# Kernel tuning notes

Measured on AMD Instinct MI355X. Metric: run time of the kernel, lower is better.

Reference implementation:

```python
import jax, jax.numpy as jnp
import numpy as np

SCORE_THRESHOLD = 0.5
GRID = 512  # spatial extent per axis; batch in {0,1} so keys fit int32
SENTINEL = np.int32(2 ** 30)  # larger than any real key (< 2**28)


def _encode(coords):
    # coords: [N,4] int32 (batch, x, y, z) -> unique int32 key
    c = coords.astype(jnp.int32)
    return ((c[:, 0] * GRID + c[:, 1]) * GRID + c[:, 2]) * GRID + c[:, 3]


def _decode_np(k):
    z = k % GRID; k = k // GRID
    y = k % GRID; k = k // GRID
    x = k % GRID; b = k // GRID
    return np.stack([b, x, y, z], axis=1).astype(np.int32)


def setup_inputs() -> dict:
    rng = np.random.default_rng(0)
    Nx, Nm, Dx = 2_000_000, 2_000_000, 16
    # draw unique coordinate keys (MinkowskiEngine coords are unique per tensor)
    keys = np.unique(rng.integers(0, 2 * GRID ** 3, size=3 * Nx, dtype=np.int64)).astype(np.int32)
    rng.shuffle(keys)
    x_keys = keys[:Nx]
    m_keys = np.concatenate([x_keys[: Nm // 2], keys[Nx: Nx + Nm - Nm // 2]])
    rng.shuffle(m_keys)
    key = jax.random.key(0)
    k1, k2 = jax.random.split(key)
    return {
        "x_C": jnp.asarray(_decode_np(x_keys)),
        "x_F": jax.random.normal(k1, (Nx, Dx), dtype=jnp.float32),
        "m_C": jnp.asarray(_decode_np(m_keys)),
        "m_F": jax.random.uniform(k2, (Nm, 1), dtype=jnp.float32),
    }


def _gather_on_union(keys, feats, union_keys):
    # scatter each tensor's features onto the union coordinate set (zeros elsewhere)
    n = keys.shape[0]
    order = jnp.argsort(keys)
    ks = keys[order]
    fs = feats[order]
    pos = jnp.searchsorted(ks, union_keys)
    pc = jnp.clip(pos, 0, n - 1)
    found = (pos < n) & (ks[pc] == union_keys)
    return jnp.where(found[:, None], fs[pc], jnp.zeros((), feats.dtype))


def reference(x_C, x_F, m_C, m_F):
    Nx, Nm = x_F.shape[0], m_F.shape[0]
    xk = _encode(x_C)
    mk = _encode(m_C)
    # coordinate union (ME sparse-tensor addition); fixed size Nx+Nm, padded w/ sentinel
    uk = jnp.unique(jnp.concatenate([xk, mk]), size=Nx + Nm, fill_value=SENTINEL)
    xf = _gather_on_union(xk, x_F, uk)   # x features on union coords  [Nu, Dx]
    mf = _gather_on_union(mk, m_F, uk)   # mask scores on union coords [Nu, 1]
    # target = score above threshold AND x has any positive feature at this coord
    target = (mf[:, 0] > SCORE_THRESHOLD) & (xf > 0).any(axis=1)
    # prune expressed as fixed-shape masking (padding rows have target=False)
    return xf * target[:, None].astype(xf.dtype)
```

## Files before the change

kernel.cpp:

```cpp
#include <hip/hip_runtime.h>
#include <hip/hip_bf16.h>
#include <stdint.h>

#define KEYSPACE     (1u << 28)
#define NBUCKET      2048u
#define BUCKET_KEYS  (KEYSPACE / NBUCKET)
#define BUCKET_WORDS (BUCKET_KEYS / 16u)
#define BUCKET_CAP   4096u
#define EPB          16384
#define UMASK        0x55555555u
#define RECS_CAP     1024u

__device__ __forceinline__ uint32_t encode4(int4 c) {
    return ((((uint32_t)c.x * 512u + (uint32_t)c.y) * 512u + (uint32_t)c.z) * 512u) + (uint32_t)c.w;
}

__global__ __launch_bounds__(256) void bin_keys(const int* __restrict__ xC,
                                                const int* __restrict__ mC,
                                                const float* __restrict__ mF,
                                                uint2* __restrict__ barr,
                                                uint32_t* __restrict__ bcnt,
                                                int Nx, int Nm) {
    __shared__ uint32_t hist[NBUCKET];
    __shared__ uint32_t base[NBUCKET];
    int t = threadIdx.x;
    int total = Nx + Nm;
    int start = blockIdx.x * EPB;
    int end = min(start + EPB, total);

    for (int q = t; q < (int)NBUCKET; q += 256) hist[q] = 0u;
    __syncthreads();

    for (int e = start + t; e < end; e += 256) {
        uint32_t k = (e < Nx) ? encode4(reinterpret_cast<const int4*>(xC)[e])
                              : encode4(reinterpret_cast<const int4*>(mC)[e - Nx]);
        atomicAdd(&hist[k >> 17], 1u);
    }
    __syncthreads();

    for (int q = t; q < (int)NBUCKET; q += 256) {
        uint32_t h = hist[q];
        base[q] = h ? atomicAdd(&bcnt[q], h) : 0u;
        hist[q] = 0u;
    }
    __syncthreads();

    for (int e = start + t; e < end; e += 256) {
        uint32_t k; uint2 pl;
        if (e < Nx) {
            k = encode4(reinterpret_cast<const int4*>(xC)[e]);
            pl.x = (k & (BUCKET_KEYS - 1u)) | (1u << 18);
            pl.y = (uint32_t)e;
        } else {
            int j = e - Nx;
            k = encode4(reinterpret_cast<const int4*>(mC)[j]);
            pl.x = (k & (BUCKET_KEYS - 1u)) | ((mF[j] > 0.5f) ? (1u << 17) : 0u);
            pl.y = 0u;
        }
        uint32_t b = k >> 17;
        uint32_t pos = base[b] + atomicAdd(&hist[b], 1u);
        barr[(size_t)b * BUCKET_CAP + pos] = pl;
    }
}

__global__ __launch_bounds__(256) void build_bucket(const uint2* __restrict__ barr,
                                                    const uint32_t* __restrict__ bcnt,
                                                    uint2* __restrict__ records,
                                                    uint32_t* __restrict__ rcount,
                                                    uint32_t* __restrict__ Btot) {
    __shared__ uint32_t bmp[BUCKET_WORDS];
    __shared__ uint32_t gpre[512];
    __shared__ uint32_t sdata[256];
    __shared__ uint2 recs[RECS_CAP];
    __shared__ uint32_t nrec, rbase;
    int t = threadIdx.x;
    uint32_t b = blockIdx.x;

    {
        uint4 z = make_uint4(0u, 0u, 0u, 0u);
        uint4* bz = reinterpret_cast<uint4*>(bmp);
        for (int q = t; q < (int)(BUCKET_WORDS / 4u); q += 256) bz[q] = z;
    }
    __syncthreads();

    uint32_t n = bcnt[b];
    const uint2* ba = barr + (size_t)b * BUCKET_CAP;

    for (uint32_t e = t; e < n; e += 256u) {
        uint32_t pl = ba[e].x;
        uint32_t off = pl & (BUCKET_KEYS - 1u);
        uint32_t bits = 1u | (((pl >> 17) & 1u) << 1);
        atomicOr(&bmp[off >> 4], bits << ((off & 15u) * 2u));
    }
    __syncthreads();

    uint32_t c0 = 0u, c1 = 0u;
    {
        const uint32_t* w0 = bmp + (2 * t) * 16;
        const uint32_t* w1 = bmp + (2 * t + 1) * 16;
#pragma unroll
        for (int q = 0; q < 16; ++q) c0 += __popc(w0[q] & UMASK);
#pragma unroll
        for (int q = 0; q < 16; ++q) c1 += __popc(w1[q] & UMASK);
    }
    uint32_t s = c0 + c1;
    sdata[t] = s;
    __syncthreads();
    for (int off = 1; off < 256; off <<= 1) {
        uint32_t tmp = (t >= off) ? sdata[t - off] : 0u;
        __syncthreads();
        sdata[t] += tmp;
        __syncthreads();
    }
    uint32_t ex = sdata[t] - s;
    gpre[2 * t] = ex;
    gpre[2 * t + 1] = ex + c0;
    if (t == 255) Btot[b] = sdata[255];
    if (t == 0) nrec = 0u;
    __syncthreads();

    for (uint32_t e = t; e < n; e += 256u) {
        uint2 pe = ba[e];
        if (!(pe.x & (1u << 18))) continue;
        uint32_t off = pe.x & (BUCKET_KEYS - 1u);
        uint32_t w = off >> 4;
        uint32_t j2 = (off & 15u) * 2u;
        uint32_t word = bmp[w];
        if (!((word >> (j2 + 1u)) & 1u)) continue;
        uint32_t g = off >> 8;
        uint32_t r = gpre[g];
        for (uint32_t q = g << 4; q < w; ++q) r += __popc(bmp[q] & UMASK);
        r += __popc(word & UMASK & ((1u << j2) - 1u));
        uint32_t pos = atomicAdd(&nrec, 1u);
        if (pos < RECS_CAP) recs[pos] = make_uint2(pe.y, (b << 17) | r);
    }
    __syncthreads();

    if (t == 0) rbase = atomicAdd(rcount, min(nrec, RECS_CAP));
    __syncthreads();
    uint32_t n2 = min(nrec, RECS_CAP);
    for (uint32_t q = t; q < n2; q += 256u) records[rbase + q] = recs[q];
}

__global__ __launch_bounds__(1024) void scan_top(const uint32_t* __restrict__ Btot,
                                                 uint32_t* __restrict__ Boff) {
    __shared__ uint32_t sdata[1024];
    int t = threadIdx.x;
    uint32_t v0 = Btot[2 * t], v1 = Btot[2 * t + 1];
    uint32_t s = v0 + v1;
    sdata[t] = s;
    __syncthreads();
    for (int off = 1; off < 1024; off <<= 1) {
        uint32_t tmp = (t >= off) ? sdata[t - off] : 0u;
        __syncthreads();
        sdata[t] += tmp;
        __syncthreads();
    }
    uint32_t ex = sdata[t] - s;
    Boff[2 * t] = ex;
    Boff[2 * t + 1] = ex + v0;
}

__global__ __launch_bounds__(256) void gather_rows(const uint2* __restrict__ records,
                                                   const uint32_t* __restrict__ rcount,
                                                   const uint32_t* __restrict__ Boff,
                                                   const float* __restrict__ xF,
                                                   float* __restrict__ out) {
    uint32_t i = blockIdx.x * blockDim.x + threadIdx.x;
    if (i >= *rcount) return;
    uint2 rec = records[i];
    uint32_t row = rec.x;
    uint32_t r = Boff[rec.y >> 17] + (rec.y & (BUCKET_KEYS - 1u));

    const float4* f = reinterpret_cast<const float4*>(xF + (size_t)row * 16u);
    float4 f0 = f[0], f1 = f[1], f2 = f[2], f3 = f[3];
    bool any =
        (f0.x > 0.f) | (f0.y > 0.f) | (f0.z > 0.f) | (f0.w > 0.f) |
        (f1.x > 0.f) | (f1.y > 0.f) | (f1.z > 0.f) | (f1.w > 0.f) |
        (f2.x > 0.f) | (f2.y > 0.f) | (f2.z > 0.f) | (f2.w > 0.f) |
        (f3.x > 0.f) | (f3.y > 0.f) | (f3.z > 0.f) | (f3.w > 0.f);
    if (!any) return;

    float4* o = reinterpret_cast<float4*>(out + (size_t)r * 16u);
    o[0] = f0; o[1] = f1; o[2] = f2; o[3] = f3;
}

extern "C" void kernel_launch(void* const* d_in, const int* in_sizes, int n_in,
                              void* d_out, int out_size, void* d_ws, size_t ws_size,
                              hipStream_t stream) {
    const int* xC = (const int*)d_in[0];
    const float* xF = (const float*)d_in[1];
    const int* mC = (const int*)d_in[2];
    const float* mF = (const float*)d_in[3];
    float* out = (float*)d_out;

    int Nx = in_sizes[1] / 16;
    int Nm = in_sizes[3];
    int total = Nx + Nm;

    uint8_t* ws = (uint8_t*)d_ws;
    uint2*    barr    = (uint2*)(ws);
    uint2*    records = (uint2*)(ws + (size_t)64 * 1024 * 1024);
    uint32_t* bcnt    = (uint32_t*)(ws + (size_t)80 * 1024 * 1024);
    uint32_t* rcount  = (uint32_t*)(ws + (size_t)80 * 1024 * 1024 + 8192);
    uint32_t* Btot    = (uint32_t*)(ws + (size_t)80 * 1024 * 1024 + 12288);
    uint32_t* Boff    = (uint32_t*)(ws + (size_t)80 * 1024 * 1024 + 20480);

    hipMemsetAsync(out, 0, (size_t)out_size * sizeof(float), stream);
    hipMemsetAsync(bcnt, 0, 8192 + 4, stream);

    bin_keys<<<(total + EPB - 1) / EPB, 256, 0, stream>>>(xC, mC, mF, barr, bcnt, Nx, Nm);
    build_bucket<<<NBUCKET, 256, 0, stream>>>(barr, bcnt, records, rcount, Btot);
    scan_top<<<1, 1024, 0, stream>>>(Btot, Boff);
    gather_rows<<<(Nx + 255) / 256, 256, 0, stream>>>(records, rcount, Boff, xF, out);
}
```

Measured before the change: 547.3 us.

## Fuse all stages into one cooperative kernel with grid syncs

```diff
diff --git a/kernel.cpp b/kernel.cpp
--- a/kernel.cpp
+++ b/kernel.cpp
@@ -1,51 +1,68 @@
 #include <hip/hip_runtime.h>
-#include <hip/hip_bf16.h>
+#include <hip/hip_cooperative_groups.h>
 #include <stdint.h>
+
+namespace cg = cooperative_groups;
 
 #define KEYSPACE     (1u << 28)
 #define NBUCKET      2048u
 #define BUCKET_KEYS  (KEYSPACE / NBUCKET)
 #define BUCKET_WORDS (BUCKET_KEYS / 16u)
 #define BUCKET_CAP   4096u
-#define EPB          16384
 #define UMASK        0x55555555u
 #define RECS_CAP     1024u
+#define NBLK         512
+#define NTHR         256
+#define BPB          ((int)NBUCKET / NBLK)
 
 __device__ __forceinline__ uint32_t encode4(int4 c) {
     return ((((uint32_t)c.x * 512u + (uint32_t)c.y) * 512u + (uint32_t)c.z) * 512u) + (uint32_t)c.w;
 }
 
-__global__ __launch_bounds__(256) void bin_keys(const int* __restrict__ xC,
-                                                const int* __restrict__ mC,
-                                                const float* __restrict__ mF,
-                                                uint2* __restrict__ barr,
-                                                uint32_t* __restrict__ bcnt,
-                                                int Nx, int Nm) {
+__global__ __launch_bounds__(NTHR) void fused(const int* __restrict__ xC,
+                                              const float* __restrict__ xF,
+                                              const int* __restrict__ mC,
+                                              const float* __restrict__ mF,
+                                              float* __restrict__ out,
+                                              uint2* __restrict__ barr,
+                                              uint32_t* __restrict__ bcnt,
+                                              uint32_t* __restrict__ rcount,
+                                              uint32_t* __restrict__ Btot,
+                                              uint32_t* __restrict__ Boff,
+                                              uint2* __restrict__ records,
+                                              int Nx, int Nm, uint32_t out4) {
     __shared__ uint32_t hist[NBUCKET];
-    __shared__ uint32_t base[NBUCKET];
+    __shared__ uint32_t base_[NBUCKET];
+    __shared__ uint32_t bmp[BUCKET_WORDS];
+    __shared__ uint32_t gpre[512];
+    __shared__ uint32_t sdata[NTHR];
+    __shared__ uint2    recs[RECS_CAP];
+    __shared__ uint32_t nrec, rbase;
+
+    cg::grid_group grid = cg::this_grid();
     int t = threadIdx.x;
+    int blk = blockIdx.x;
     int total = Nx + Nm;
-    int start = blockIdx.x * EPB;
-    int end = min(start + EPB, total);
-
-    for (int q = t; q < (int)NBUCKET; q += 256) hist[q] = 0u;
+
+    int epb = (total + NBLK - 1) / NBLK;
+    int start = blk * epb;
+    int end = min(start + epb, total);
+
+    for (int q = t; q < (int)NBUCKET; q += NTHR) hist[q] = 0u;
     __syncthreads();
-
-    for (int e = start + t; e < end; e += 256) {
+    for (int e = start + t; e < end; e += NTHR) {
         uint32_t k = (e < Nx) ? encode4(reinterpret_cast<const int4*>(xC)[e])
                               : encode4(reinterpret_cast<const int4*>(mC)[e - Nx]);
         atomicAdd(&hist[k >> 17], 1u);
     }
     __syncthreads();
-
-    for (int q = t; q < (int)NBUCKET; q += 256) {
+    for (int q = t; q < (int)NBUCKET; q += NTHR) {
         uint32_t h = hist[q];
-        base[q] = h ? atomicAdd(&bcnt[q], h) : 0u;
+        base_[q] = h ? atomicAdd(&bcnt[q], h) : 0u;
         hist[q] = 0u;
     }
     __syncthreads();
-
-    for (int e = start + t; e < end; e += 256) {
+    for (int e = start + t; e < end; e += NTHR) {
         uint32_t k; uint2 pl;
         if (e < Nx) {
             k = encode4(reinterpret_cast<const int4*>(xC)[e]);
@@ -58,131 +75,118 @@
             pl.y = 0u;
         }
         uint32_t b = k >> 17;
-        uint32_t pos = base[b] + atomicAdd(&hist[b], 1u);
+        uint32_t pos = base_[b] + atomicAdd(&hist[b], 1u);
         barr[(size_t)b * BUCKET_CAP + pos] = pl;
     }
-}
-
-__global__ __launch_bounds__(256) void build_bucket(const uint2* __restrict__ barr,
-                                                    const uint32_t* __restrict__ bcnt,
-                                                    uint2* __restrict__ records,
-                                                    uint32_t* __restrict__ rcount,
-                                                    uint32_t* __restrict__ Btot) {
-    __shared__ uint32_t bmp[BUCKET_WORDS];
-    __shared__ uint32_t gpre[512];
-    __shared__ uint32_t sdata[256];
-    __shared__ uint2 recs[RECS_CAP];
-    __shared__ uint32_t nrec, rbase;
-    int t = threadIdx.x;
-    uint32_t b = blockIdx.x;
-
+    grid.sync();
+
+    for (int bk = 0; bk < BPB; ++bk) {
+        uint32_t b = (uint32_t)(blk * BPB + bk);
+        {
+            uint4 z = make_uint4(0u, 0u, 0u, 0u);
+            uint4* bz = reinterpret_cast<uint4*>(bmp);
+            for (int q = t; q < (int)(BUCKET_WORDS / 4u); q += NTHR) bz[q] = z;
+        }
+        __syncthreads();
+        uint32_t n = bcnt[b];
+        const uint2* ba = barr + (size_t)b * BUCKET_CAP;
+        for (uint32_t e = t; e < n; e += NTHR) {
+            uint32_t pl = ba[e].x;
+            uint32_t off = pl & (BUCKET_KEYS - 1u);
+            uint32_t bits = 1u | (((pl >> 17) & 1u) << 1);
+            atomicOr(&bmp[off >> 4], bits << ((off & 15u) * 2u));
+        }
+        __syncthreads();
+
+        uint32_t c0 = 0u, c1 = 0u;
+        {
+            const uint32_t* w0 = bmp + (2 * t) * 16;
+            const uint32_t* w1 = bmp + (2 * t + 1) * 16;
+#pragma unroll
+            for (int q = 0; q < 16; ++q) c0 += __popc(w0[q] & UMASK);
+#pragma unroll
+            for (int q = 0; q < 16; ++q) c1 += __popc(w1[q] & UMASK);
+        }
+        uint32_t s = c0 + c1;
+        sdata[t] = s;
+        __syncthreads();
+        for (int off = 1; off < NTHR; off <<= 1) {
+            uint32_t tmp = (t >= off) ? sdata[t - off] : 0u;
+            __syncthreads();
+            sdata[t] += tmp;
+            __syncthreads();
+        }
+        uint32_t ex = sdata[t] - s;
+        gpre[2 * t] = ex;
+        gpre[2 * t + 1] = ex + c0;
+        if (t == NTHR - 1) Btot[b] = sdata[NTHR - 1];
+        if (t == 0) nrec = 0u;
+        __syncthreads();
+
+        for (uint32_t e = t; e < n; e += NTHR) {
+            uint2 pe = ba[e];
+            if (!(pe.x & (1u << 18))) continue;
+            uint32_t off = pe.x & (BUCKET_KEYS - 1u);
+            uint32_t w = off >> 4;
+            uint32_t j2 = (off & 15u) * 2u;
+            uint32_t word = bmp[w];
+            if (!((word >> (j2 + 1u)) & 1u)) continue;
+            uint32_t g = off >> 8;
+            uint32_t r = gpre[g];
+            for (uint32_t q = g << 4; q < w; ++q) r += __popc(bmp[q] & UMASK);
+            r += __popc(word & UMASK & ((1u << j2) - 1u));
+            uint32_t pos = atomicAdd(&nrec, 1u);
+            if (pos < RECS_CAP) recs[pos] = make_uint2(pe.y, (b << 17) | r);
+        }
+        __syncthreads();
+        if (t == 0) rbase = atomicAdd(rcount, min(nrec, RECS_CAP));
+        __syncthreads();
+        uint32_t n2 = min(nrec, RECS_CAP);
+        for (uint32_t q = t; q < n2; q += NTHR) records[rbase + q] = recs[q];
+        __syncthreads();
+    }
+    grid.sync();
+
+    if (blk == 0) {
+        uint32_t v[8]; uint32_t s = 0u;
+#pragma unroll
+        for (int q = 0; q < 8; ++q) { v[q] = Btot[t * 8 + q]; s += v[q]; }
+        sdata[t] = s;
+        __syncthreads();
+        for (int off = 1; off < NTHR; off <<= 1) {
+            uint32_t tmp = (t >= off) ? sdata[t - off] : 0u;
+            __syncthreads();
+            sdata[t] += tmp;
+            __syncthreads();
+        }
+        uint32_t ex = sdata[t] - s;
+#pragma unroll
+        for (int q = 0; q < 8; ++q) { Boff[t * 8 + q] = ex; ex += v[q]; }
+    }
     {
         uint4 z = make_uint4(0u, 0u, 0u, 0u);
-        uint4* bz = reinterpret_cast<uint4*>(bmp);
-        for (int q = t; q < (int)(BUCKET_WORDS / 4u); q += 256) bz[q] = z;
-    }
-    __syncthreads();
-
-    uint32_t n = bcnt[b];
-    const uint2* ba = barr + (size_t)b * BUCKET_CAP;
-
-    for (uint32_t e = t; e < n; e += 256u) {
-        uint32_t pl = ba[e].x;
-        uint32_t off = pl & (BUCKET_KEYS - 1u);
-        uint32_t bits = 1u | (((pl >> 17) & 1u) << 1);
-        atomicOr(&bmp[off >> 4], bits << ((off & 15u) * 2u));
-    }
-    __syncthreads();
-
-    uint32_t c0 = 0u, c1 = 0u;
-    {
-        const uint32_t* w0 = bmp + (2 * t) * 16;
-        const uint32_t* w1 = bmp + (2 * t + 1) * 16;
-#pragma unroll
-        for (int q = 0; q < 16; ++q) c0 += __popc(w0[q] & UMASK);
-#pragma unroll
-        for (int q = 0; q < 16; ++q) c1 += __popc(w1[q] & UMASK);
-    }
-    uint32_t s = c0 + c1;
-    sdata[t] = s;
-    __syncthreads();
-    for (int off = 1; off < 256; off <<= 1) {
-        uint32_t tmp = (t >= off) ? sdata[t - off] : 0u;
-        __syncthreads();
-        sdata[t] += tmp;
-        __syncthreads();
-    }
-    uint32_t ex = sdata[t] - s;
-    gpre[2 * t] = ex;
-    gpre[2 * t + 1] = ex + c0;
-    if (t == 255) Btot[b] = sdata[255];
-    if (t == 0) nrec = 0u;
-    __syncthreads();
-
-    for (uint32_t e = t; e < n; e += 256u) {
-        uint2 pe = ba[e];
-        if (!(pe.x & (1u << 18))) continue;
-        uint32_t off = pe.x & (BUCKET_KEYS - 1u);
-        uint32_t w = off >> 4;
-        uint32_t j2 = (off & 15u) * 2u;
-        uint32_t word = bmp[w];
-        if (!((word >> (j2 + 1u)) & 1u)) continue;
-        uint32_t g = off >> 8;
-        uint32_t r = gpre[g];
-        for (uint32_t q = g << 4; q < w; ++q) r += __popc(bmp[q] & UMASK);
-        r += __popc(word & UMASK & ((1u << j2) - 1u));
-        uint32_t pos = atomicAdd(&nrec, 1u);
-        if (pos < RECS_CAP) recs[pos] = make_uint2(pe.y, (b << 17) | r);
-    }
-    __syncthreads();
-
-    if (t == 0) rbase = atomicAdd(rcount, min(nrec, RECS_CAP));
-    __syncthreads();
-    uint32_t n2 = min(nrec, RECS_CAP);
-    for (uint32_t q = t; q < n2; q += 256u) records[rbase + q] = recs[q];
-}
-
-__global__ __launch_bounds__(1024) void scan_top(const uint32_t* __restrict__ Btot,
-                                                 uint32_t* __restrict__ Boff) {
-    __shared__ uint32_t sdata[1024];
-    int t = threadIdx.x;
-    uint32_t v0 = Btot[2 * t], v1 = Btot[2 * t + 1];
-    uint32_t s = v0 + v1;
-    sdata[t] = s;
-    __syncthreads();
-    for (int off = 1; off < 1024; off <<= 1) {
-        uint32_t tmp = (t >= off) ? sdata[t - off] : 0u;
-        __syncthreads();
-        sdata[t] += tmp;
-        __syncthreads();
-    }
-    uint32_t ex = sdata[t] - s;
-    Boff[2 * t] = ex;
-    Boff[2 * t + 1] = ex + v0;
-}
-
-__global__ __launch_bounds__(256) void gather_rows(const uint2* __restrict__ records,
-                                                   const uint32_t* __restrict__ rcount,
-                                                   const uint32_t* __restrict__ Boff,
-                                                   const float* __restrict__ xF,
-                                                   float* __restrict__ out) {
-    uint32_t i = blockIdx.x * blockDim.x + threadIdx.x;
-    if (i >= *rcount) return;
-    uint2 rec = records[i];
-    uint32_t row = rec.x;
-    uint32_t r = Boff[rec.y >> 17] + (rec.y & (BUCKET_KEYS - 1u));
-
-    const float4* f = reinterpret_cast<const float4*>(xF + (size_t)row * 16u);
-    float4 f0 = f[0], f1 = f[1], f2 = f[2], f3 = f[3];
-    bool any =
-        (f0.x > 0.f) | (f0.y > 0.f) | (f0.z > 0.f) | (f0.w > 0.f) |
-        (f1.x > 0.f) | (f1.y > 0.f) | (f1.z > 0.f) | (f1.w > 0.f) |
-        (f2.x > 0.f) | (f2.y > 0.f) | (f2.z > 0.f) | (f2.w > 0.f) |
-        (f3.x > 0.f) | (f3.y > 0.f) | (f3.z > 0.f) | (f3.w > 0.f);
-    if (!any) return;
-
-    float4* o = reinterpret_cast<float4*>(out + (size_t)r * 16u);
-    o[0] = f0; o[1] = f1; o[2] = f2; o[3] = f3;
+        uint4* o4 = reinterpret_cast<uint4*>(out);
+        uint32_t gtid = (uint32_t)(blk * NTHR + t);
+        for (uint32_t q = gtid; q < out4; q += (uint32_t)(NBLK * NTHR)) o4[q] = z;
+    }
+    grid.sync();
+
+    uint32_t nr = *rcount;
+    uint32_t gtid = (uint32_t)(blk * NTHR + t);
+    for (uint32_t i = gtid; i < nr; i += (uint32_t)(NBLK * NTHR)) {
+        uint2 rec = records[i];
+        uint32_t r = Boff[rec.y >> 17] + (rec.y & (BUCKET_KEYS - 1u));
+        const float4* f = reinterpret_cast<const float4*>(xF + (size_t)rec.x * 16u);
+        float4 f0 = f[0], f1 = f[1], f2 = f[2], f3 = f[3];
+        bool any =
+            (f0.x > 0.f) | (f0.y > 0.f) | (f0.z > 0.f) | (f0.w > 0.f) |
+            (f1.x > 0.f) | (f1.y > 0.f) | (f1.z > 0.f) | (f1.w > 0.f) |
+            (f2.x > 0.f) | (f2.y > 0.f) | (f2.z > 0.f) | (f2.w > 0.f) |
+            (f3.x > 0.f) | (f3.y > 0.f) | (f3.z > 0.f) | (f3.w > 0.f);
+        if (!any) continue;
+        float4* o = reinterpret_cast<float4*>(out + (size_t)r * 16u);
+        o[0] = f0; o[1] = f1; o[2] = f2; o[3] = f3;
+    }
 }
 
 extern "C" void kernel_launch(void* const* d_in, const int* in_sizes, int n_in,
@@ -196,7 +200,7 @@
 
     int Nx = in_sizes[1] / 16;
     int Nm = in_sizes[3];
-    int total = Nx + Nm;
+    uint32_t out4 = (uint32_t)(out_size / 4);
 
     uint8_t* ws = (uint8_t*)d_ws;
     uint2*    barr    = (uint2*)(ws);
@@ -206,11 +210,12 @@
     uint32_t* Btot    = (uint32_t*)(ws + (size_t)80 * 1024 * 1024 + 12288);
     uint32_t* Boff    = (uint32_t*)(ws + (size_t)80 * 1024 * 1024 + 20480);
 
-    hipMemsetAsync(out, 0, (size_t)out_size * sizeof(float), stream);
     hipMemsetAsync(bcnt, 0, 8192 + 4, stream);
 
-    bin_keys<<<(total + EPB - 1) / EPB, 256, 0, stream>>>(xC, mC, mF, barr, bcnt, Nx, Nm);
-    build_bucket<<<NBUCKET, 256, 0, stream>>>(barr, bcnt, records, rcount, Btot);
-    scan_top<<<1, 1024, 0, stream>>>(Btot, Boff);
-    gather_rows<<<(Nx + 255) / 256, 256, 0, stream>>>(records, rcount, Boff, xF, out);
+    void* args[] = {(void*)&xC, (void*)&xF, (void*)&mC, (void*)&mF, (void*)&out,
+                    (void*)&barr, (void*)&bcnt, (void*)&rcount, (void*)&Btot,
+                    (void*)&Boff, (void*)&records, (void*)&Nx, (void*)&Nm,
+                    (void*)&out4};
+    hipLaunchCooperativeKernel((const void*)fused, dim3(NBLK), dim3(NTHR),
+                               args, 0, stream);
 }
```

After: 737.8 us. 1.35x slower.

## Fuse output zeroing into binning kernel, swizzle bitmap LDS, halve elements per block

Applied to the files above, without the earlier changes.

```diff
diff --git a/kernel.cpp b/kernel.cpp
--- a/kernel.cpp
+++ b/kernel.cpp
@@ -1,5 +1,4 @@
 #include <hip/hip_runtime.h>
-#include <hip/hip_bf16.h>
 #include <stdint.h>
 
 #define KEYSPACE     (1u << 28)
@@ -7,25 +6,36 @@
 #define BUCKET_KEYS  (KEYSPACE / NBUCKET)
 #define BUCKET_WORDS (BUCKET_KEYS / 16u)
 #define BUCKET_CAP   4096u
-#define EPB          16384
+#define EPB          8192
 #define UMASK        0x55555555u
 #define RECS_CAP     1024u
 
 __device__ __forceinline__ uint32_t encode4(int4 c) {
     return ((((uint32_t)c.x * 512u + (uint32_t)c.y) * 512u + (uint32_t)c.z) * 512u) + (uint32_t)c.w;
 }
-
-__global__ __launch_bounds__(256) void bin_keys(const int* __restrict__ xC,
+__device__ __forceinline__ uint32_t swz(uint32_t w) { return w ^ ((w >> 5) & 31u); }
+
+__global__ __launch_bounds__(256) void bin_zero(const int* __restrict__ xC,
                                                 const int* __restrict__ mC,
                                                 const float* __restrict__ mF,
                                                 uint2* __restrict__ barr,
                                                 uint32_t* __restrict__ bcnt,
-                                                int Nx, int Nm) {
+                                                float* __restrict__ out,
+                                                uint32_t out4, int Nx, int Nm) {
     __shared__ uint32_t hist[NBUCKET];
-    __shared__ uint32_t base[NBUCKET];
+    __shared__ uint32_t base_[NBUCKET];
     int t = threadIdx.x;
+    int blk = blockIdx.x;
+    uint32_t nthr = gridDim.x * 256u;
+
+    {
+        uint4 z = make_uint4(0u, 0u, 0u, 0u);
+        uint4* o4 = reinterpret_cast<uint4*>(out);
+        for (uint32_t q = (uint32_t)blk * 256u + t; q < out4; q += nthr) o4[q] = z;
+    }
+
     int total = Nx + Nm;
-    int start = blockIdx.x * EPB;
+    int start = blk * EPB;
     int end = min(start + EPB, total);
 
     for (int q = t; q < (int)NBUCKET; q += 256) hist[q] = 0u;
@@ -40,7 +50,7 @@
 
     for (int q = t; q < (int)NBUCKET; q += 256) {
         uint32_t h = hist[q];
-        base[q] = h ? atomicAdd(&bcnt[q], h) : 0u;
+        base_[q] = h ? atomicAdd(&bcnt[q], h) : 0u;
         hist[q] = 0u;
     }
     __syncthreads();
@@ -58,7 +68,7 @@
             pl.y = 0u;
         }
         uint32_t b = k >> 17;
-        uint32_t pos = base[b] + atomicAdd(&hist[b], 1u);
+        uint32_t pos = base_[b] + atomicAdd(&hist[b], 1u);
         barr[(size_t)b * BUCKET_CAP + pos] = pl;
     }
 }
@@ -90,18 +100,17 @@
         uint32_t pl = ba[e].x;
         uint32_t off = pl & (BUCKET_KEYS - 1u);
         uint32_t bits = 1u | (((pl >> 17) & 1u) << 1);
-        atomicOr(&bmp[off >> 4], bits << ((off & 15u) * 2u));
+        atomicOr(&bmp[swz(off >> 4)], bits << ((off & 15u) * 2u));
     }
     __syncthreads();
 
     uint32_t c0 = 0u, c1 = 0u;
     {
-        const uint32_t* w0 = bmp + (2 * t) * 16;
-        const uint32_t* w1 = bmp + (2 * t + 1) * 16;
+        uint32_t b0 = 32u * (uint32_t)t, b1 = b0 + 16u;
 #pragma unroll
-        for (int q = 0; q < 16; ++q) c0 += __popc(w0[q] & UMASK);
+        for (uint32_t q = 0; q < 16u; ++q) c0 += __popc(bmp[swz(b0 + q)] & UMASK);
 #pragma unroll
-        for (int q = 0; q < 16; ++q) c1 += __popc(w1[q] & UMASK);
+        for (uint32_t q = 0; q < 16u; ++q) c1 += __popc(bmp[swz(b1 + q)] & UMASK);
     }
     uint32_t s = c0 + c1;
     sdata[t] = s;
@@ -125,11 +134,11 @@
         uint32_t off = pe.x & (BUCKET_KEYS - 1u);
         uint32_t w = off >> 4;
         uint32_t j2 = (off & 15u) * 2u;
-        uint32_t word = bmp[w];
+        uint32_t word = bmp[swz(w)];
         if (!((word >> (j2 + 1u)) & 1u)) continue;
         uint32_t g = off >> 8;
         uint32_t r = gpre[g];
-        for (uint32_t q = g << 4; q < w; ++q) r += __popc(bmp[q] & UMASK);
+        for (uint32_t q = g << 4; q < w; ++q) r += __popc(bmp[swz(q)] & UMASK);
         r += __popc(word & UMASK & ((1u << j2) - 1u));
         uint32_t pos = atomicAdd(&nrec, 1u);
         if (pos < RECS_CAP) recs[pos] = make_uint2(pe.y, (b << 17) | r);
@@ -169,10 +178,9 @@
     uint32_t i = blockIdx.x * blockDim.x + threadIdx.x;
     if (i >= *rcount) return;
     uint2 rec = records[i];
-    uint32_t row = rec.x;
     uint32_t r = Boff[rec.y >> 17] + (rec.y & (BUCKET_KEYS - 1u));
 
-    const float4* f = reinterpret_cast<const float4*>(xF + (size_t)row * 16u);
+    const float4* f = reinterpret_cast<const float4*>(xF + (size_t)rec.x * 16u);
     float4 f0 = f[0], f1 = f[1], f2 = f[2], f3 = f[3];
     bool any =
         (f0.x > 0.f) | (f0.y > 0.f) | (f0.z > 0.f) | (f0.w > 0.f) |
@@ -197,6 +205,7 @@
     int Nx = in_sizes[1] / 16;
     int Nm = in_sizes[3];
     int total = Nx + Nm;
+    uint32_t out4 = (uint32_t)(out_size / 4);
 
     uint8_t* ws = (uint8_t*)d_ws;
     uint2*    barr    = (uint2*)(ws);
@@ -206,10 +215,10 @@
     uint32_t* Btot    = (uint32_t*)(ws + (size_t)80 * 1024 * 1024 + 12288);
     uint32_t* Boff    = (uint32_t*)(ws + (size_t)80 * 1024 * 1024 + 20480);
 
-    hipMemsetAsync(out, 0, (size_t)out_size * sizeof(float), stream);
     hipMemsetAsync(bcnt, 0, 8192 + 4, stream);
 
-    bin_keys<<<(total + EPB - 1) / EPB, 256, 0, stream>>>(xC, mC, mF, barr, bcnt, Nx, Nm);
+    int nbin = (total + EPB - 1) / EPB;
+    bin_zero<<<nbin, 256, 0, stream>>>(xC, mC, mF, barr, bcnt, out, out4, Nx, Nm);
     build_bucket<<<NBUCKET, 256, 0, stream>>>(barr, bcnt, records, rcount, Btot);
     scan_top<<<1, 1024, 0, stream>>>(Btot, Boff);
     gather_rows<<<(Nx + 255) / 256, 256, 0, stream>>>(records, rcount, Boff, xF, out);
```

After: 522.8 us. 1.05x faster.
